# Kernel tuning notes

Measured on AMD Instinct MI355X. Metric: run time of the kernel, lower is better.

The kernel has to match this reference:

```python
import jax, jax.numpy as jnp
import numpy as np
import math

# Model hyperparameters (SchNet defaults)
H = 128        # hidden_channels
F = 128        # num_filters
G = 50         # num_gaussians
CUT = 6.0      # cutoff (Angstrom)
L_INT = 3      # num_interactions
# Graph scale
N_MOL = 512    # molecules
APM = 32       # atoms per molecule
N = N_MOL * APM
BOX = 10.0     # side of cubic box per molecule


def _ssp(x):
    # ShiftedSoftplus
    return jax.nn.softplus(x) - math.log(2.0)


def setup_inputs() -> dict:
    rng = np.random.default_rng(0)
    pos = rng.uniform(0.0, BOX, (N_MOL, APM, 3)).astype(np.float32)
    # radius graph within each molecule (faithful to radius_graph_custom,
    # precomputed here because edge count is data-dependent)
    srcs, dsts = [], []
    for m in range(N_MOL):
        p = pos[m]
        dm = np.linalg.norm(p[:, None, :] - p[None, :, :], axis=-1)
        mask = dm <= CUT
        np.fill_diagonal(mask, False)
        s, t = np.nonzero(mask)
        srcs.append(s + m * APM)
        dsts.append(t + m * APM)
    edge_index = np.stack([np.concatenate(srcs), np.concatenate(dsts)]).astype(np.int32)
    pos = pos.reshape(N, 3)
    batch = np.repeat(np.arange(N_MOL, dtype=np.int32), APM)
    z = rng.integers(1, 100, N).astype(np.int32)

    key = jax.random.key(0)
    ks = jax.random.split(key, 16)
    s = 0.1
    nrm = lambda k, shp: (jax.random.normal(k, shp, dtype=jnp.float32) * s)
    return {
        "z": jnp.asarray(z),
        "pos": jnp.asarray(pos),
        "batch": jnp.asarray(batch),
        "edge_index": jnp.asarray(edge_index),
        "emb": nrm(ks[0], (100, H)),
        "mlp_w1": nrm(ks[1], (L_INT, G, F)),
        "mlp_b1": jnp.zeros((L_INT, F), jnp.float32),
        "mlp_w2": nrm(ks[2], (L_INT, F, F)),
        "mlp_b2": jnp.zeros((L_INT, F), jnp.float32),
        "cf1_w": nrm(ks[3], (L_INT, H, F)),
        "cf2_w": nrm(ks[4], (L_INT, F, H)),
        "cf2_b": jnp.zeros((L_INT, H), jnp.float32),
        "lin_w": nrm(ks[5], (L_INT, H, H)),
        "lin_b": jnp.zeros((L_INT, H), jnp.float32),
        "out1_w": nrm(ks[6], (H, H // 2)),
        "out1_b": jnp.zeros((H // 2,), jnp.float32),
        "out2_w": nrm(ks[7], (H // 2, 1)),
        "out2_b": jnp.zeros((1,), jnp.float32),
    }


def reference(z, pos, batch, edge_index, emb,
              mlp_w1, mlp_b1, mlp_w2, mlp_b2,
              cf1_w, cf2_w, cf2_b, lin_w, lin_b,
              out1_w, out1_b, out2_w, out2_b):
    src, dst = edge_index[0], edge_index[1]
    # edge_weight = euclidean distance (== cdist[src, dst])
    d = jnp.sqrt(jnp.sum((pos[src] - pos[dst]) ** 2, axis=-1))  # [E]
    # GaussianSmearing
    offs = jnp.linspace(0.0, CUT, G)
    coeff = -0.5 / (CUT / (G - 1)) ** 2
    edge_attr = jnp.exp(coeff * (d[:, None] - offs[None, :]) ** 2)  # [E, G]
    # cosine cutoff
    Ccut = 0.5 * (jnp.cos(d * math.pi / CUT) + 1.0)  # [E]

    h = emb[z]  # [N, H]
    for l in range(L_INT):
        # edge filter MLP with cutoff
        W = _ssp(edge_attr @ mlp_w1[l] + mlp_b1[l]) @ mlp_w2[l] + mlp_b2[l]  # [E, F]
        W = W * Ccut[:, None]
        # CFConv: lin1 -> gather x_j -> multiply -> scatter-add to dst -> lin2
        msg = (h @ cf1_w[l])[src] * W                                # [E, F]
        agg = jax.ops.segment_sum(msg, dst, num_segments=N)          # [N, F]
        v = agg @ cf2_w[l] + cf2_b[l]                                # [N, H]
        v = _ssp(v)
        v = v @ lin_w[l] + lin_b[l]
        h = h + v  # residual

    h = _ssp(h @ out1_w + out1_b)
    h = h @ out2_w + out2_b                                          # [N, 1]
    out = jax.ops.segment_sum(h, batch, num_segments=N_MOL)          # [N_MOL, 1]
    return out
```

## Files before the change

### kernel.cpp

```cpp
#include <hip/hip_runtime.h>
#include <hip/hip_bf16.h>
#include <hip/hip_fp16.h>
#include <math.h>

#define NATOMS 16384
#define NMOL   512
#define APM    32
#define GDIM   50
#define KTAB   4096

#define STRH 132
#define STRA 136

typedef __attribute__((ext_vector_type(8))) short   short8;
typedef __attribute__((ext_vector_type(4))) float   floatx4;

__device__ __forceinline__ float ssp(float x) {
    float e = __expf(-fabsf(x));
    return fmaxf(x, 0.0f) + __logf(1.0f + e) - 0.69314718055994531f;
}

__device__ __forceinline__ unsigned short f2bf(float x) {
    union { float f; unsigned int u; } v; v.f = x;
    unsigned int lsb = (v.u >> 16) & 1u;
    v.u += 0x7fffu + lsb;
    return (unsigned short)(v.u >> 16);
}

__device__ __forceinline__ unsigned short f2h(float x) {
    __half h = __float2half(x);
    unsigned short u;
    __builtin_memcpy(&u, &h, 2);
    return u;
}

__device__ __forceinline__ unsigned int pk2bf(float a, float b) {
    __hip_bfloat162 h = __float22bfloat162_rn(make_float2(a, b));
    unsigned int u;
    __builtin_memcpy(&u, &h, 4);
    return u;
}

#define KW2 136
#define NTILE (KTAB / 64)

#define N_WTALL  147456
#define N_OUT1   8192
#define N_W1T    24576
#define N_W2T    49152
#define WB_ELEMS (N_WTALL + N_OUT1 + N_W1T + N_W2T)
#define WB_BLOCKS (WB_ELEMS / 256)

__global__ __launch_bounds__(256) void setup_a_kernel(
    const float* __restrict__ pos,
    unsigned* __restrict__ koG,
    const float* __restrict__ cf1, const float* __restrict__ cf2,
    const float* __restrict__ lin, const float* __restrict__ out1,
    const float* __restrict__ w1_, const float* __restrict__ w2_,
    unsigned short* __restrict__ Wtall, unsigned short* __restrict__ Wmlp,
    unsigned short* __restrict__ Tt)
{
    const int b = blockIdx.x;
    const int tid = threadIdx.x;

    __shared__ float sp[96];

    if (b < NMOL) {
        if (tid < 96) sp[tid] = pos[b * 96 + tid];
        if (b < 3 && tid < 128)
            Tt[(size_t)b * (KTAB + 1) * 128 + (size_t)KTAB * 128 + tid] = 0;
        __syncthreads();
        #pragma unroll
        for (int c4 = 0; c4 < 4; c4++) {
            int c = c4 * 256 + tid;
            int i = c >> 5, j = c & 31;
            float dx = sp[3 * i]     - sp[3 * j];
            float dy = sp[3 * i + 1] - sp[3 * j + 1];
            float dz = sp[3 * i + 2] - sp[3 * j + 2];
            float d  = sqrtf(dx * dx + dy * dy + dz * dz);
            unsigned off = (unsigned)(KTAB << 8);
            if (i != j && d <= 6.0f) {
                float u = d * (float)(KTAB - 1) / 6.0f;
                int k = min((int)(u + 0.5f), KTAB - 1);
                off = (unsigned)(k << 8);
            }
            koG[((size_t)b << 10) + c] = off;
        }
        return;
    }

    int idx = (b - NMOL) * 256 + tid;
    if (idx < N_WTALL) {
        int wi = idx >> 14, rem = idx & 16383;
        int n = rem >> 7, k = rem & 127;
        int l = wi / 3, which = wi % 3;
        const float* src = (which == 0) ? cf1 : (which == 1) ? cf2 : lin;
        Wtall[idx] = f2bf(src[(size_t)l * 16384 + k * 128 + n]);
    } else if (idx < N_WTALL + N_OUT1) {
        int q = idx - N_WTALL;
        int n = q >> 7, k = q & 127;
        Wtall[idx] = f2bf(out1[k * 64 + n]);
    } else if (idx < N_WTALL + N_OUT1 + N_W1T) {
        int q = idx - (N_WTALL + N_OUT1);
        int l = q >> 13, rem = q & 8191;
        int n = rem >> 6, k = rem & 63;
        Wmlp[q] = (k < GDIM) ? f2bf(w1_[(size_t)l * GDIM * 128 + k * 128 + n]) : 0;
    } else {
        int q = idx - (N_WTALL + N_OUT1 + N_W1T);
        int l = q >> 14, rem = q & 16383;
        int n = rem >> 7, k = rem & 127;
        Wmlp[N_W1T + q] = f2bf(w2_[(size_t)l * 16384 + k * 128 + n]);
    }
}

__global__ __launch_bounds__(256) void setup_b_kernel(
    const unsigned short* __restrict__ Wmlp,
    const float* __restrict__ b1_, const float* __restrict__ b2_,
    unsigned short* __restrict__ Tt)
{
    __shared__ unsigned short s_t[64 * KW2];

    const int tt = blockIdx.x;
    const int l  = tt / NTILE;
    const int bx = tt % NTILE;
    const unsigned short* W1g = Wmlp + (size_t)l * 8192;
    const unsigned short* W2g = Wmlp + N_W1T + (size_t)l * 16384;
    const float* b1 = b1_ + (size_t)l * 128;
    const float* b2 = b2_ + (size_t)l * 128;
    unsigned short* Tg = Tt + (size_t)l * (KTAB + 1) * 128;

    const int tid  = threadIdx.x;
    const int lane = tid & 63;
    const int w    = tid >> 6;
    const int l15  = lane & 15;
    const int quad = lane >> 4;

    float b1v[8], b2v[8];
    #pragma unroll
    for (int nt = 0; nt < 8; nt++) {
        b1v[nt] = b1[nt * 16 + l15];
        b2v[nt] = b2[nt * 16 + l15];
    }

    const float hstep = 6.0f / (float)(KTAB - 1);
    const float step  = 6.0f / 49.0f;
    const float coeff = -0.5f / (step * step);
    const float pioc  = 3.14159265358979323846f / 6.0f;
    const int k0 = bx * 64;
    const float dm = (float)(k0 + w * 16 + l15) * hstep;

    floatx4 acc1[8];
    #pragma unroll
    for (int nt = 0; nt < 8; nt++) acc1[nt] = (floatx4){0.f, 0.f, 0.f, 0.f};
    #pragma unroll
    for (int ks = 0; ks < 2; ks++) {
        unsigned int ap[4];
        #pragma unroll
        for (int jj = 0; jj < 4; jj++) {
            int g0 = ks * 32 + quad * 8 + 2 * jj;
            float d0 = dm - (float)g0 * step;
            float d1 = dm - (float)(g0 + 1) * step;
            float v0 = (g0 < GDIM)     ? __expf(coeff * d0 * d0) : 0.0f;
            float v1 = (g0 + 1 < GDIM) ? __expf(coeff * d1 * d1) : 0.0f;
            ap[jj] = pk2bf(v0, v1);
        }
        short8 af;
        __builtin_memcpy(&af, ap, 16);
        #pragma unroll
        for (int nt = 0; nt < 8; nt++) {
            short8 bfg = *(const short8*)&W1g[(nt * 16 + l15) * 64 + ks * 32 + quad * 8];
            acc1[nt] = __builtin_amdgcn_mfma_f32_16x16x32_bf16(af, bfg, acc1[nt], 0, 0, 0);
        }
    }

    #pragma unroll
    for (int nt = 0; nt < 8; nt++) {
        #pragma unroll
        for (int r = 0; r < 4; r++) {
            int row = w * 16 + quad * 4 + r;
            s_t[row * KW2 + nt * 16 + l15] = f2bf(ssp(acc1[nt][r] + b1v[nt]));
        }
    }

    floatx4 acc2[8];
    #pragma unroll
    for (int nt = 0; nt < 8; nt++) acc2[nt] = (floatx4){0.f, 0.f, 0.f, 0.f};
    #pragma unroll
    for (int ks = 0; ks < 4; ks++) {
        short8 af = *(const short8*)&s_t[(w * 16 + l15) * KW2 + ks * 32 + quad * 8];
        #pragma unroll
        for (int nt = 0; nt < 8; nt++) {
            short8 bfg = *(const short8*)&W2g[(nt * 16 + l15) * 128 + ks * 32 + quad * 8];
            acc2[nt] = __builtin_amdgcn_mfma_f32_16x16x32_bf16(af, bfg, acc2[nt], 0, 0, 0);
        }
    }

    #pragma unroll
    for (int nt = 0; nt < 8; nt++) {
        #pragma unroll
        for (int r = 0; r < 4; r++) {
            int row = w * 16 + quad * 4 + r;
            float d = (float)(k0 + row) * hstep;
            float cut = 0.5f * (__cosf(d * pioc) + 1.0f);
            Tg[(size_t)(k0 + row) * 128 + nt * 16 + l15] = f2h((acc2[nt][r] + b2v[nt]) * cut);
        }
    }
}

__global__ __launch_bounds__(512, 4) void fused_schnet_kernel(
    const int* __restrict__ z, const float* __restrict__ emb,
    const unsigned* __restrict__ koG,
    const unsigned short* __restrict__ Tt,
    const unsigned short* __restrict__ Wtall,
    const float* __restrict__ cf2_b, const float* __restrict__ lin_b,
    const float* __restrict__ out1_b, const float* __restrict__ out2_w,
    const float* __restrict__ out2_b,
    float* __restrict__ out)
{
    __shared__ float s_h[32 * STRH];
    __shared__ float s_hx[32 * 128];
    __shared__ unsigned short s_agg[32 * STRA];
    __shared__ unsigned int s_ko[32 * 32];
    __shared__ float s_red;
    unsigned short* s_t = (unsigned short*)s_hx;

    const int tid  = threadIdx.x;
    const int lane = tid & 63;
    const int w    = tid >> 6;
    const int l15  = lane & 15;
    const int quad = lane >> 4;
    const int r16  = (w & 1) * 16;
    const int c32  = (w >> 1) * 32;
    const int B0   = blockIdx.x * 32;

    const unsigned lOff = (unsigned)(lane << 2);

    for (int i = tid; i < 32 * 128; i += 512) {
        int row = i >> 7, col = i & 127;
        s_h[row * STRH + col] = emb[(size_t)z[B0 + row] * 128 + col];
    }
    for (int i = tid; i < 1024; i += 512)
        s_ko[i] = koG[((size_t)blockIdx.x << 10) + i];
    if (tid == 0) s_red = 0.0f;

    __syncthreads();

    const unsigned short* WtO = Wtall + 9 * 16384;

#define KO_RFL(KO, SC)                                                        \
    _Pragma("unroll")                                                         \
    for (int i = 0; i < 4; i++) {                                             \
        uint4 ka = *(const uint4*)&s_ko[(((w << 2) + i) << 5) + ((SC) << 3)]; \
        uint4 kb = *(const uint4*)&s_ko[(((w << 2) + i) << 5) + ((SC) << 3) + 4]; \
        KO[i][0] = __builtin_amdgcn_readfirstlane(ka.x);                      \
        KO[i][1] = __builtin_amdgcn_readfirstlane(ka.y);                      \
        KO[i][2] = __builtin_amdgcn_readfirstlane(ka.z);                      \
        KO[i][3] = __builtin_amdgcn_readfirstlane(ka.w);                      \
        KO[i][4] = __builtin_amdgcn_readfirstlane(kb.x);                      \
        KO[i][5] = __builtin_amdgcn_readfirstlane(kb.y);                      \
        KO[i][6] = __builtin_amdgcn_readfirstlane(kb.z);                      \
        KO[i][7] = __builtin_amdgcn_readfirstlane(kb.w);                      \
    }
#define TP_LOAD(TP, KO)                                                       \
    _Pragma("unroll")                                                         \
    for (int i = 0; i < 4; i++) {                                             \
        _Pragma("unroll")                                                     \
        for (int j = 0; j < 8; j++)                                           \
            TP[i][j] = *(const unsigned*)(TlB + KO[i][j] + lOff);             \
    }
#define FMA_CHUNK(TP, SC)                                                     \
    _Pragma("unroll")                                                         \
    for (int j = 0; j < 8; j++) {                                             \
        float2 hv = *(const float2*)&s_hx[((((SC) << 3) + j) << 7) + (lane << 1)]; \
        _Pragma("unroll")                                                     \
        for (int i = 0; i < 4; i++) {                                         \
            unsigned t = TP[i][j];                                            \
            asm("v_fma_mix_f32 %0, %1, %2, %0 op_sel:[0,0,0] op_sel_hi:[1,0,0]" \
                : "+v"(a0[i]) : "v"(t), "v"(hv.x));                           \
            asm("v_fma_mix_f32 %0, %1, %2, %0 op_sel:[1,0,0] op_sel_hi:[1,0,0]" \
                : "+v"(a1[i]) : "v"(t), "v"(hv.y));                           \
        }                                                                     \
    }

    for (int l = 0; l < 3; l++) {
        const unsigned short* W1 = Wtall + (size_t)(l * 3 + 0) * 16384;
        const unsigned short* W2 = Wtall + (size_t)(l * 3 + 1) * 16384;
        const unsigned short* W3 = Wtall + (size_t)(l * 3 + 2) * 16384;
        const char* TlB = (const char*)(Tt + (size_t)l * (KTAB + 1) * 128);

        floatx4 acc[2];
        #pragma unroll
        for (int nt = 0; nt < 2; nt++) acc[nt] = (floatx4){0.f, 0.f, 0.f, 0.f};
        #pragma unroll
        for (int ks = 0; ks < 4; ks++) {
            const float* hp = &s_h[(r16 + l15) * STRH + ks * 32 + quad * 8];
            float4 xa = *(const float4*)hp;
            float4 xb = *(const float4*)(hp + 4);
            unsigned int ap[4];
            ap[0] = pk2bf(xa.x, xa.y); ap[1] = pk2bf(xa.z, xa.w);
            ap[2] = pk2bf(xb.x, xb.y); ap[3] = pk2bf(xb.z, xb.w);
            short8 af;
            __builtin_memcpy(&af, ap, 16);
            #pragma unroll
            for (int nt = 0; nt < 2; nt++) {
                short8 bfg = *(const short8*)&W1[(size_t)(c32 + nt * 16 + l15) * 128 + ks * 32 + quad * 8];
                acc[nt] = __builtin_amdgcn_mfma_f32_16x16x32_bf16(af, bfg, acc[nt], 0, 0, 0);
            }
        }
        #pragma unroll
        for (int nt = 0; nt < 2; nt++) {
            #pragma unroll
            for (int r = 0; r < 4; r++)
                s_hx[(r16 + quad * 4 + r) * 128 + c32 + nt * 16 + l15] = acc[nt][r];
        }

        __syncthreads();

        {
            float a0[4], a1[4];
            #pragma unroll
            for (int i = 0; i < 4; i++) { a0[i] = 0.0f; a1[i] = 0.0f; }

            unsigned koA[4][8], koB[4][8], tpA[4][8], tpB[4][8];
            KO_RFL(koA, 0)
            TP_LOAD(tpA, koA)

            KO_RFL(koB, 1)
            TP_LOAD(tpB, koB)
            FMA_CHUNK(tpA, 0)

            KO_RFL(koA, 2)
            TP_LOAD(tpA, koA)
            FMA_CHUNK(tpB, 1)

            KO_RFL(koB, 3)
            TP_LOAD(tpB, koB)
            FMA_CHUNK(tpA, 2)

            FMA_CHUNK(tpB, 3)

            #pragma unroll
            for (int i = 0; i < 4; i++)
                *(unsigned*)&s_agg[((w << 2) + i) * STRA + (lane << 1)] = pk2bf(a0[i], a1[i]);
        }

        __syncthreads();

        float bva[2], bvb[2];
        #pragma unroll
        for (int nt = 0; nt < 2; nt++) {
            bva[nt] = cf2_b[l * 128 + c32 + nt * 16 + l15];
            bvb[nt] = lin_b[l * 128 + c32 + nt * 16 + l15];
        }
        #pragma unroll
        for (int nt = 0; nt < 2; nt++) acc[nt] = (floatx4){0.f, 0.f, 0.f, 0.f};
        #pragma unroll
        for (int ks = 0; ks < 4; ks++) {
            short8 af = *(const short8*)&s_agg[(r16 + l15) * STRA + ks * 32 + quad * 8];
            #pragma unroll
            for (int nt = 0; nt < 2; nt++) {
                short8 bfg = *(const short8*)&W2[(size_t)(c32 + nt * 16 + l15) * 128 + ks * 32 + quad * 8];
                acc[nt] = __builtin_amdgcn_mfma_f32_16x16x32_bf16(af, bfg, acc[nt], 0, 0, 0);
            }
        }
        #pragma unroll
        for (int nt = 0; nt < 2; nt++) {
            #pragma unroll
            for (int r = 0; r < 4; r++) {
                int row = r16 + quad * 4 + r;
                s_t[row * STRA + c32 + nt * 16 + l15] = f2bf(ssp(acc[nt][r] + bva[nt]));
            }
        }

        __syncthreads();

        #pragma unroll
        for (int nt = 0; nt < 2; nt++) acc[nt] = (floatx4){0.f, 0.f, 0.f, 0.f};
        #pragma unroll
        for (int ks = 0; ks < 4; ks++) {
            short8 af = *(const short8*)&s_t[(r16 + l15) * STRA + ks * 32 + quad * 8];
            #pragma unroll
            for (int nt = 0; nt < 2; nt++) {
                short8 bfg = *(const short8*)&W3[(size_t)(c32 + nt * 16 + l15) * 128 + ks * 32 + quad * 8];
                acc[nt] = __builtin_amdgcn_mfma_f32_16x16x32_bf16(af, bfg, acc[nt], 0, 0, 0);
            }
        }
        #pragma unroll
        for (int nt = 0; nt < 2; nt++) {
            #pragma unroll
            for (int r = 0; r < 4; r++) {
                int row = r16 + quad * 4 + r;
                s_h[row * STRH + c32 + nt * 16 + l15] += acc[nt][r] + bvb[nt];
            }
        }
        __syncthreads();
    }

    const int c16 = (w >> 1) * 16;
    floatx4 ha = (floatx4){0.f, 0.f, 0.f, 0.f};
    #pragma unroll
    for (int ks = 0; ks < 4; ks++) {
        const float* hp = &s_h[(r16 + l15) * STRH + ks * 32 + quad * 8];
        float4 xa = *(const float4*)hp;
        float4 xb = *(const float4*)(hp + 4);
        unsigned int ap[4];
        ap[0] = pk2bf(xa.x, xa.y); ap[1] = pk2bf(xa.z, xa.w);
        ap[2] = pk2bf(xb.x, xb.y); ap[3] = pk2bf(xb.z, xb.w);
        short8 af;
        __builtin_memcpy(&af, ap, 16);
        short8 bfg = *(const short8*)&WtO[(size_t)(c16 + l15) * 128 + ks * 32 + quad * 8];
        ha = __builtin_amdgcn_mfma_f32_16x16x32_bf16(af, bfg, ha, 0, 0, 0);
    }
    float part = 0.0f;
    {
        float b1o = out1_b[c16 + l15];
        float o2  = out2_w[c16 + l15];
        #pragma unroll
        for (int r = 0; r < 4; r++)
            part += ssp(ha[r] + b1o) * o2;
    }
    #pragma unroll
    for (int off = 32; off > 0; off >>= 1) part += __shfl_down(part, off);
    if (lane == 0) atomicAdd(&s_red, part);
    __syncthreads();
    if (tid == 0) out[blockIdx.x] = s_red + 32.0f * out2_b[0];

#undef KO_RFL
#undef TP_LOAD
#undef FMA_CHUNK
}

extern "C" void kernel_launch(void* const* d_in, const int* in_sizes, int n_in,
                              void* d_out, int out_size, void* d_ws, size_t ws_size,
                              hipStream_t stream)
{
    const int*   z      = (const int*)d_in[0];
    const float* pos    = (const float*)d_in[1];
    const float* emb    = (const float*)d_in[4];
    const float* mlp_w1 = (const float*)d_in[5];
    const float* mlp_b1 = (const float*)d_in[6];
    const float* mlp_w2 = (const float*)d_in[7];
    const float* mlp_b2 = (const float*)d_in[8];
    const float* cf1_w  = (const float*)d_in[9];
    const float* cf2_w  = (const float*)d_in[10];
    const float* cf2_b  = (const float*)d_in[11];
    const float* lin_w  = (const float*)d_in[12];
    const float* lin_b  = (const float*)d_in[13];
    const float* out1_w = (const float*)d_in[14];
    const float* out1_b = (const float*)d_in[15];
    const float* out2_w = (const float*)d_in[16];
    const float* out2_b = (const float*)d_in[17];

    char* p = (char*)d_ws;
    unsigned* koG = (unsigned*)p;                 p += (size_t)NMOL * 1024 * 4;
    unsigned short* Tt = (unsigned short*)p;      p += (size_t)3 * (KTAB + 1) * 128 * 2;
    unsigned short* Wtall = (unsigned short*)p;   p += ((size_t)(N_WTALL + N_OUT1) * 2 + 63) & ~63ULL;
    unsigned short* Wmlp = (unsigned short*)p;

    setup_a_kernel<<<NMOL + WB_BLOCKS, 256, 0, stream>>>(
        pos, koG, cf1_w, cf2_w, lin_w, out1_w, mlp_w1, mlp_w2,
        Wtall, Wmlp, Tt);

    setup_b_kernel<<<NTILE * 3, 256, 0, stream>>>(
        Wmlp, mlp_b1, mlp_b2, Tt);

    fused_schnet_kernel<<<NMOL, 512, 0, stream>>>(
        z, emb, koG, Tt, Wtall,
        cf2_b, lin_b, out1_b, out2_w, out2_b, (float*)d_out);
}
```

Baseline: 157.9 us.

## Double threads per molecule block to split GEMM and gather work across 16 waves

Raises the fused kernel's block from 512 to 1024 threads. Each wave now owns one 16-column MFMA tile instead of two, and two destination atoms instead of four in the gather-FMA aggregation. The output head is restricted to the first 8 waves. This aims to raise latency hiding and parallelism with only 512 blocks on the device, at the cost of more per-block synchronisation overhead and less independent work per wave to overlap memory loads.

After: 161.4 us. +2.2%, slower.

```diff
diff --git a/kernel.cpp b/kernel.cpp
--- a/kernel.cpp
+++ b/kernel.cpp
@@ -207,7 +207,7 @@
     }
 }
 
-__global__ __launch_bounds__(512, 4) void fused_schnet_kernel(
+__global__ __launch_bounds__(1024, 8) void fused_schnet_kernel(
     const int* __restrict__ z, const float* __restrict__ emb,
     const unsigned* __restrict__ koG,
     const unsigned short* __restrict__ Tt,
@@ -230,17 +230,16 @@
     const int l15  = lane & 15;
     const int quad = lane >> 4;
     const int r16  = (w & 1) * 16;
-    const int c32  = (w >> 1) * 32;
+    const int c16  = (w >> 1) * 16;
     const int B0   = blockIdx.x * 32;
 
     const unsigned lOff = (unsigned)(lane << 2);
 
-    for (int i = tid; i < 32 * 128; i += 512) {
+    for (int i = tid; i < 32 * 128; i += 1024) {
         int row = i >> 7, col = i & 127;
         s_h[row * STRH + col] = emb[(size_t)z[B0 + row] * 128 + col];
     }
-    for (int i = tid; i < 1024; i += 512)
-        s_ko[i] = koG[((size_t)blockIdx.x << 10) + i];
+    if (tid < 1024) s_ko[tid] = koG[((size_t)blockIdx.x << 10) + tid];
     if (tid == 0) s_red = 0.0f;
 
     __syncthreads();
@@ -249,9 +248,9 @@
 
 #define KO_RFL(KO, SC)                                                        \
     _Pragma("unroll")                                                         \
-    for (int i = 0; i < 4; i++) {                                             \
-        uint4 ka = *(const uint4*)&s_ko[(((w << 2) + i) << 5) + ((SC) << 3)]; \
-        uint4 kb = *(const uint4*)&s_ko[(((w << 2) + i) << 5) + ((SC) << 3) + 4]; \
+    for (int i = 0; i < 2; i++) {                                             \
+        uint4 ka = *(const uint4*)&s_ko[(((w << 1) + i) << 5) + ((SC) << 3)]; \
+        uint4 kb = *(const uint4*)&s_ko[(((w << 1) + i) << 5) + ((SC) << 3) + 4]; \
         KO[i][0] = __builtin_amdgcn_readfirstlane(ka.x);                      \
         KO[i][1] = __builtin_amdgcn_readfirstlane(ka.y);                      \
         KO[i][2] = __builtin_amdgcn_readfirstlane(ka.z);                      \
@@ -263,7 +262,7 @@
     }
 #define TP_LOAD(TP, KO)                                                       \
     _Pragma("unroll")                                                         \
-    for (int i = 0; i < 4; i++) {                                             \
+    for (int i = 0; i < 2; i++) {                                             \
         _Pragma("unroll")                                                     \
         for (int j = 0; j < 8; j++)                                           \
             TP[i][j] = *(const unsigned*)(TlB + KO[i][j] + lOff);             \
@@ -273,7 +272,7 @@
     for (int j = 0; j < 8; j++) {                                             \
         float2 hv = *(const float2*)&s_hx[((((SC) << 3) + j) << 7) + (lane << 1)]; \
         _Pragma("unroll")                                                     \
-        for (int i = 0; i < 4; i++) {                                         \
+        for (int i = 0; i < 2; i++) {                                         \
             unsigned t = TP[i][j];                                            \
             asm("v_fma_mix_f32 %0, %1, %2, %0 op_sel:[0,0,0] op_sel_hi:[1,0,0]" \
                 : "+v"(a0[i]) : "v"(t), "v"(hv.x));                           \
@@ -288,9 +287,7 @@
         const unsigned short* W3 = Wtall + (size_t)(l * 3 + 2) * 16384;
         const char* TlB = (const char*)(Tt + (size_t)l * (KTAB + 1) * 128);
 
-        floatx4 acc[2];
-        #pragma unroll
-        for (int nt = 0; nt < 2; nt++) acc[nt] = (floatx4){0.f, 0.f, 0.f, 0.f};
+        floatx4 acc = (floatx4){0.f, 0.f, 0.f, 0.f};
         #pragma unroll
         for (int ks = 0; ks < 4; ks++) {
             const float* hp = &s_h[(r16 + l15) * STRH + ks * 32 + quad * 8];
@@ -301,27 +298,21 @@
             ap[2] = pk2bf(xb.x, xb.y); ap[3] = pk2bf(xb.z, xb.w);
             short8 af;
             __builtin_memcpy(&af, ap, 16);
+            short8 bfg = *(const short8*)&W1[(size_t)(c16 + l15) * 128 + ks * 32 + quad * 8];
+            acc = __builtin_amdgcn_mfma_f32_16x16x32_bf16(af, bfg, acc, 0, 0, 0);
+        }
+        #pragma unroll
+        for (int r = 0; r < 4; r++)
+            s_hx[(r16 + quad * 4 + r) * 128 + c16 + l15] = acc[r];
+
+        __syncthreads();
+
+        {
+            float a0[2], a1[2];
             #pragma unroll
-            for (int nt = 0; nt < 2; nt++) {
-                short8 bfg = *(const short8*)&W1[(size_t)(c32 + nt * 16 + l15) * 128 + ks * 32 + quad * 8];
-                acc[nt] = __builtin_amdgcn_mfma_f32_16x16x32_bf16(af, bfg, acc[nt], 0, 0, 0);
-            }
-        }
-        #pragma unroll
-        for (int nt = 0; nt < 2; nt++) {
-            #pragma unroll
-            for (int r = 0; r < 4; r++)
-                s_hx[(r16 + quad * 4 + r) * 128 + c32 + nt * 16 + l15] = acc[nt][r];
-        }
-
-        __syncthreads();
-
-        {
-            float a0[4], a1[4];
-            #pragma unroll
-            for (int i = 0; i < 4; i++) { a0[i] = 0.0f; a1[i] = 0.0f; }
-
-            unsigned koA[4][8], koB[4][8], tpA[4][8], tpB[4][8];
+            for (int i = 0; i < 2; i++) { a0[i] = 0.0f; a1[i] = 0.0f; }
+
+            unsigned koA[2][8], koB[2][8], tpA[2][8], tpB[2][8];
             KO_RFL(koA, 0)
             TP_LOAD(tpA, koA)
 
@@ -340,88 +331,70 @@
             FMA_CHUNK(tpB, 3)
 
             #pragma unroll
-            for (int i = 0; i < 4; i++)
-                *(unsigned*)&s_agg[((w << 2) + i) * STRA + (lane << 1)] = pk2bf(a0[i], a1[i]);
+            for (int i = 0; i < 2; i++)
+                *(unsigned*)&s_agg[((w << 1) + i) * STRA + (lane << 1)] = pk2bf(a0[i], a1[i]);
         }
 
         __syncthreads();
 
-        float bva[2], bvb[2];
-        #pragma unroll
-        for (int nt = 0; nt < 2; nt++) {
-            bva[nt] = cf2_b[l * 128 + c32 + nt * 16 + l15];
-            bvb[nt] = lin_b[l * 128 + c32 + nt * 16 + l15];
-        }
-        #pragma unroll
-        for (int nt = 0; nt < 2; nt++) acc[nt] = (floatx4){0.f, 0.f, 0.f, 0.f};
+        float bva = cf2_b[l * 128 + c16 + l15];
+        float bvb = lin_b[l * 128 + c16 + l15];
+        acc = (floatx4){0.f, 0.f, 0.f, 0.f};
         #pragma unroll
         for (int ks = 0; ks < 4; ks++) {
             short8 af = *(const short8*)&s_agg[(r16 + l15) * STRA + ks * 32 + quad * 8];
-            #pragma unroll
-            for (int nt = 0; nt < 2; nt++) {
-                short8 bfg = *(const short8*)&W2[(size_t)(c32 + nt * 16 + l15) * 128 + ks * 32 + quad * 8];
-                acc[nt] = __builtin_amdgcn_mfma_f32_16x16x32_bf16(af, bfg, acc[nt], 0, 0, 0);
-            }
-        }
-        #pragma unroll
-        for (int nt = 0; nt < 2; nt++) {
-            #pragma unroll
-            for (int r = 0; r < 4; r++) {
-                int row = r16 + quad * 4 + r;
-                s_t[row * STRA + c32 + nt * 16 + l15] = f2bf(ssp(acc[nt][r] + bva[nt]));
-            }
+            short8 bfg = *(const short8*)&W2[(size_t)(c16 + l15) * 128 + ks * 32 + quad * 8];
+            acc = __builtin_amdgcn_mfma_f32_16x16x32_bf16(af, bfg, acc, 0, 0, 0);
+        }
+        #pragma unroll
+        for (int r = 0; r < 4; r++) {
+            int row = r16 + quad * 4 + r;
+            s_t[row * STRA + c16 + l15] = f2bf(ssp(acc[r] + bva));
         }
 
         __syncthreads();
 
-        #pragma unroll
-        for (int nt = 0; nt < 2; nt++) acc[nt] = (floatx4){0.f, 0.f, 0.f, 0.f};
+        acc = (floatx4){0.f, 0.f, 0.f, 0.f};
         #pragma unroll
         for (int ks = 0; ks < 4; ks++) {
             short8 af = *(const short8*)&s_t[(r16 + l15) * STRA + ks * 32 + quad * 8];
-            #pragma unroll
-            for (int nt = 0; nt < 2; nt++) {
-                short8 bfg = *(const short8*)&W3[(size_t)(c32 + nt * 16 + l15) * 128 + ks * 32 + quad * 8];
-                acc[nt] = __builtin_amdgcn_mfma_f32_16x16x32_bf16(af, bfg, acc[nt], 0, 0, 0);
-            }
-        }
-        #pragma unroll
-        for (int nt = 0; nt < 2; nt++) {
-            #pragma unroll
-            for (int r = 0; r < 4; r++) {
-                int row = r16 + quad * 4 + r;
-                s_h[row * STRH + c32 + nt * 16 + l15] += acc[nt][r] + bvb[nt];
-            }
+            short8 bfg = *(const short8*)&W3[(size_t)(c16 + l15) * 128 + ks * 32 + quad * 8];
+            acc = __builtin_amdgcn_mfma_f32_16x16x32_bf16(af, bfg, acc, 0, 0, 0);
+        }
+        #pragma unroll
+        for (int r = 0; r < 4; r++) {
+            int row = r16 + quad * 4 + r;
+            s_h[row * STRH + c16 + l15] += acc[r] + bvb;
         }
         __syncthreads();
     }
 
-    const int c16 = (w >> 1) * 16;
-    floatx4 ha = (floatx4){0.f, 0.f, 0.f, 0.f};
-    #pragma unroll
-    for (int ks = 0; ks < 4; ks++) {
-        const float* hp = &s_h[(r16 + l15) * STRH + ks * 32 + quad * 8];
-        float4 xa = *(const float4*)hp;
-        float4 xb = *(const float4*)(hp + 4);
-        unsigned int ap[4];
-        ap[0] = pk2bf(xa.x, xa.y); ap[1] = pk2bf(xa.z, xa.w);
-        ap[2] = pk2bf(xb.x, xb.y); ap[3] = pk2bf(xb.z, xb.w);
-        short8 af;
-        __builtin_memcpy(&af, ap, 16);
-        short8 bfg = *(const short8*)&WtO[(size_t)(c16 + l15) * 128 + ks * 32 + quad * 8];
-        ha = __builtin_amdgcn_mfma_f32_16x16x32_bf16(af, bfg, ha, 0, 0, 0);
-    }
     float part = 0.0f;
-    {
-        float b1o = out1_b[c16 + l15];
-        float o2  = out2_w[c16 + l15];
+    if (w < 8) {
+        const int c16h = (w >> 1) * 16;
+        floatx4 ha = (floatx4){0.f, 0.f, 0.f, 0.f};
+        #pragma unroll
+        for (int ks = 0; ks < 4; ks++) {
+            const float* hp = &s_h[(r16 + l15) * STRH + ks * 32 + quad * 8];
+            float4 xa = *(const float4*)hp;
+            float4 xb = *(const float4*)(hp + 4);
+            unsigned int ap[4];
+            ap[0] = pk2bf(xa.x, xa.y); ap[1] = pk2bf(xa.z, xa.w);
+            ap[2] = pk2bf(xb.x, xb.y); ap[3] = pk2bf(xb.z, xb.w);
+            short8 af;
+            __builtin_memcpy(&af, ap, 16);
+            short8 bfg = *(const short8*)&WtO[(size_t)(c16h + l15) * 128 + ks * 32 + quad * 8];
+            ha = __builtin_amdgcn_mfma_f32_16x16x32_bf16(af, bfg, ha, 0, 0, 0);
+        }
+        float b1o = out1_b[c16h + l15];
+        float o2  = out2_w[c16h + l15];
         #pragma unroll
         for (int r = 0; r < 4; r++)
             part += ssp(ha[r] + b1o) * o2;
-    }
-    #pragma unroll
-    for (int off = 32; off > 0; off >>= 1) part += __shfl_down(part, off);
-    if (lane == 0) atomicAdd(&s_red, part);
+        #pragma unroll
+        for (int off = 32; off > 0; off >>= 1) part += __shfl_down(part, off);
+        if (lane == 0) atomicAdd(&s_red, part);
+    }
     __syncthreads();
     if (tid == 0) out[blockIdx.x] = s_red + 32.0f * out2_b[0];
 
@@ -464,7 +437,7 @@
     setup_b_kernel<<<NTILE * 3, 256, 0, stream>>>(
         Wmlp, mlp_b1, mlp_b2, Tt);
 
-    fused_schnet_kernel<<<NMOL, 512, 0, stream>>>(
+    fused_schnet_kernel<<<NMOL, 1024, 0, stream>>>(
         z, emb, koG, Tt, Wtall,
         cf2_b, lin_b, out1_b, out2_w, out2_b, (float*)d_out);
 }
```
